# Kernel tuning notes

Measured on AMD Instinct MI355X. Metric: run time of the kernel, lower is better.

Reference implementation:

```python
import jax, jax.numpy as jnp
import numpy as np

LEAKY_ALPHA = 0.2  # LeakyReLU negative slope from init arg `alpha`


def setup_inputs() -> dict:
    key = jax.random.key(0)
    k1, k2, k3, k4 = jax.random.split(key, 4)
    B, N, Fin, Fout = 8, 2048, 256, 256
    h = jax.random.normal(k1, (B, N, Fin), dtype=jnp.float32)
    adj = jax.random.randint(k2, (N, N), 0, 2, dtype=jnp.int32)
    W = jax.random.normal(k3, (Fin, Fout), dtype=jnp.float32) * (1.414 * (6.0 / (Fin + Fout)) ** 0.5)
    a = jax.random.normal(k4, (2 * Fout, 1), dtype=jnp.float32) * (1.414 * (6.0 / (2 * Fout + 1)) ** 0.5)
    return {"h": h, "adj": adj, "W": W, "a": a}


def reference(h, adj, W, a):
    # h: (B, N, Fin), adj: (N, N) int {0,1}, W: (Fin, Fout), a: (2*Fout, 1)
    Fout = W.shape[1]
    Wh = jnp.einsum('bnf,fo->bno', h, W)            # (B, N, Fout)
    a1 = a[:Fout, 0]                                  # attends to target node i
    a2 = a[Fout:, 0]                                  # attends to source node j
    # a^T [Wh_i || Wh_j] == (Wh_i . a1) + (Wh_j . a2); LeakyReLU applied after, as in original
    s_i = Wh @ a1                                     # (B, N)
    s_j = Wh @ a2                                     # (B, N)
    e = jax.nn.leaky_relu(s_i[:, :, None] + s_j[:, None, :], negative_slope=LEAKY_ALPHA)  # (B, N, N)
    N = Wh.shape[1]
    mask = (adj > 0) | jnp.eye(N, dtype=bool)         # adjacency + self-loops
    e = jnp.where(mask[None, :, :], e, -jnp.inf)
    attention = jax.nn.softmax(e, axis=-1)            # dropout is identity in eval
    attention = jnp.nan_to_num(attention, nan=0.0)
    h_prime = jnp.einsum('bij,bjo->bio', attention, Wh)  # (B, N, Fout)
    return jax.nn.elu(h_prime)                        # concat=True -> ELU
```

## Files before the change

### kernel.cpp

```cpp
#include <hip/hip_runtime.h>

typedef unsigned short u16;
typedef unsigned int   u32;
typedef unsigned long long u64;

typedef __bf16 bf16x8 __attribute__((ext_vector_type(8)));
typedef float  f32x4  __attribute__((ext_vector_type(4)));

#define MFMA_BF16(a,b,c) __builtin_amdgcn_mfma_f32_16x16x32_bf16((a),(b),(c),0,0,0)

__device__ __forceinline__ float bf2f(u16 u) {
    return __uint_as_float(((u32)u) << 16);
}
__device__ __forceinline__ u16 f2bf(float x) {
    u32 u = __float_as_uint(x);
    u += 0x7fffu + ((u >> 16) & 1u);
    return (u16)(u >> 16);
}
__device__ __forceinline__ float ldany(const void* p, size_t i, int f32) {
    return f32 ? ((const float*)p)[i] : bf2f(((const u16*)p)[i]);
}
__device__ __forceinline__ int detect_f32(const u32* hw) {
    u32 w = hw[threadIdx.x & 63];
    int e = (w >> 23) & 0xFF;
    u64 m = __ballot(e >= 64 && e <= 190);
    return __popcll(m) >= 32 ? 1 : 0;
}

__global__ __launch_bounds__(256) void k0(const void* __restrict__ w, const void* __restrict__ a,
                                          u16* __restrict__ wt, float* __restrict__ wa1,
                                          float* __restrict__ wa2, const u32* __restrict__ hw) {
    int f32 = detect_f32(hw);
    int k = blockIdx.x, o = threadIdx.x;
    float wv = ldany(w, (size_t)k * 256 + o, f32);
    wt[o * 256 + k] = f2bf(wv);
    float p1 = wv * ldany(a, o, f32);
    float p2 = wv * ldany(a, 256 + o, f32);
    for (int d = 32; d; d >>= 1) { p1 += __shfl_down(p1, d); p2 += __shfl_down(p2, d); }
    __shared__ float s1[4], s2[4];
    int wid = o >> 6, lane = o & 63;
    if (lane == 0) { s1[wid] = p1; s2[wid] = p2; }
    __syncthreads();
    if (o == 0) { wa1[k] = s1[0] + s1[1] + s1[2] + s1[3]; wa2[k] = s2[0] + s2[1] + s2[2] + s2[3]; }
}

__global__ __launch_bounds__(256) void k1m(const int* __restrict__ adj, u64* __restrict__ mb64) {
    int t = threadIdx.x;
    int wv = t >> 6, lane = t & 63;
    #pragma unroll
    for (int q = 0; q < 4; q++) {
        int idx = blockIdx.x * 16 + wv * 4 + q;
        int mrow = idx >> 5, c = idx & 31;
        int j = c * 64 + lane;
        bool bit = (adj[(size_t)mrow * 2048 + j] > 0) || (j == mrow);
        u64 m = __ballot(bit);
        if (lane == 0) mb64[(size_t)mrow * 32 + c] = m;
    }
}

struct __align__(16) K2LDS {
    u16 At[64 * 68];
    union { u16 Bt[256 * 68]; u16 Ct[256 * 68]; };
    float wa1s[256], wa2s[256];
    float s1[64], s2[64];
};
__global__ __launch_bounds__(256) void k2(const void* __restrict__ h, const u16* __restrict__ wt,
                                          const float* __restrict__ wa1, const float* __restrict__ wa2,
                                          u16* __restrict__ whbt,
                                          float* __restrict__ sig, float* __restrict__ sjg) {
    __shared__ K2LDS L;
    int f32 = detect_f32((const u32*)h);
    int m0 = blockIdx.x * 64;
    int b  = m0 >> 11;
    int n0 = m0 & 2047;
    int t = threadIdx.x;
    int wid = t >> 6, lane = t & 63, ln = lane & 15, qd = lane >> 4;

    L.wa1s[t] = wa1[t]; L.wa2s[t] = wa2[t];
    if (t < 64) { L.s1[t] = 0.f; L.s2[t] = 0.f; }
    __syncthreads();

    float a1lo = 0.f, a2lo = 0.f, a1hi = 0.f, a2hi = 0.f;

    f32x4 acc[4][4];
    for (int mi = 0; mi < 4; mi++)
        for (int ni = 0; ni < 4; ni++)
            acc[mi][ni] = (f32x4){0.f, 0.f, 0.f, 0.f};

    for (int c = 0; c < 4; c++) {
        int k0c = c * 64;
        for (int p = 0; p < 2; p++) {
            int r = (t >> 3) + p * 32, s = t & 7;
            float xv[8]; u16 uv[8];
            if (f32) {
                const float* src = (const float*)h + (size_t)(m0 + r) * 256 + k0c + s * 8;
                f32x4 x0 = *(const f32x4*)src;
                f32x4 x1 = *(const f32x4*)(src + 4);
                #pragma unroll
                for (int q = 0; q < 4; q++) { xv[q] = x0[q]; xv[4 + q] = x1[q]; }
                #pragma unroll
                for (int q = 0; q < 8; q++) uv[q] = f2bf(xv[q]);
            } else {
                const u16* src = (const u16*)h + (size_t)(m0 + r) * 256 + k0c + s * 8;
                *(uint4*)uv = *(const uint4*)src;
                #pragma unroll
                for (int q = 0; q < 8; q++) xv[q] = bf2f(uv[q]);
            }
            *(uint4*)&L.At[r * 68 + s * 8] = *(uint4*)uv;
            float pa = 0.f, pb = 0.f;
            #pragma unroll
            for (int q = 0; q < 8; q++) {
                pa += xv[q] * L.wa1s[k0c + s * 8 + q];
                pb += xv[q] * L.wa2s[k0c + s * 8 + q];
            }
            if (p == 0) { a1lo += pa; a2lo += pb; } else { a1hi += pa; a2hi += pb; }
        }
        for (int p = 0; p < 8; p++) {
            int f = (t >> 3) + p * 32, s = t & 7;
            *(uint4*)&L.Bt[f * 68 + s * 8] =
                *(const uint4*)(wt + (size_t)f * 256 + k0c + s * 8);
        }
        __syncthreads();
        for (int ks = 0; ks < 2; ks++) {
            bf16x8 af[4], bfr[4];
            for (int mi = 0; mi < 4; mi++)
                af[mi] = *(const bf16x8*)&L.At[(mi * 16 + ln) * 68 + ks * 32 + qd * 8];
            for (int ni = 0; ni < 4; ni++)
                bfr[ni] = *(const bf16x8*)&L.Bt[(wid * 64 + ni * 16 + ln) * 68 + ks * 32 + qd * 8];
            for (int mi = 0; mi < 4; mi++)
                for (int ni = 0; ni < 4; ni++)
                    acc[mi][ni] = MFMA_BF16(af[mi], bfr[ni], acc[mi][ni]);
        }
        __syncthreads();
    }

    atomicAdd(&L.s1[t >> 3], a1lo);        atomicAdd(&L.s2[t >> 3], a2lo);
    atomicAdd(&L.s1[(t >> 3) + 32], a1hi); atomicAdd(&L.s2[(t >> 3) + 32], a2hi);

    for (int mi = 0; mi < 4; mi++) {
        for (int ni = 0; ni < 4; ni++) {
            int f = wid * 64 + ni * 16 + ln;
            int n = mi * 16 + qd * 4;
            u16 v[4];
            for (int r = 0; r < 4; r++) v[r] = f2bf(acc[mi][ni][r]);
            *(uint2*)&L.Ct[f * 68 + n] = *(uint2*)v;
        }
    }
    __syncthreads();
    if (t < 64) { sig[m0 + t] = L.s1[t]; sjg[m0 + t] = L.s2[t]; }
    {
        int fr = t;
        size_t base = (size_t)b * 524288 + (size_t)fr * 2048 + n0;
        #pragma unroll
        for (int s = 0; s < 8; s++) {
            uint4 v = *(uint4*)&L.Ct[fr * 68 + s * 8];
            *(uint4*)(whbt + base + s * 8) = v;
        }
    }
}

__global__ __launch_bounds__(512) void k3n(const float* __restrict__ sig, const float* __restrict__ sjg,
                                           float* __restrict__ u1g, float* __restrict__ u2g,
                                           u32* __restrict__ vpackg, u16* __restrict__ sjbfg) {
    int b = blockIdx.x;
    int t = threadIdx.x;
    const float* sjb = sjg + (size_t)b * 2048;
    float mx = -3.4e38f;
    #pragma unroll
    for (int p = 0; p < 4; p++) mx = fmaxf(mx, sjb[t + p * 512]);
    for (int d = 32; d; d >>= 1) mx = fmaxf(mx, __shfl_xor(mx, d));
    __shared__ float wmax[8];
    int wid = t >> 6, lane = t & 63;
    if (lane == 0) wmax[wid] = mx;
    __syncthreads();
    float Mb = fmaxf(fmaxf(fmaxf(wmax[0], wmax[1]), fmaxf(wmax[2], wmax[3])),
                     fmaxf(fmaxf(wmax[4], wmax[5]), fmaxf(wmax[6], wmax[7])));
    #pragma unroll
    for (int p = 0; p < 4; p++) {
        int j = t + p * 512;
        float sjv = sjb[j];
        float vj  = __expf(sjv - Mb);
        float v2j = __expf(0.2f * (sjv - Mb));
        vpackg[b * 2048 + j] = (u32)f2bf(vj) | ((u32)f2bf(v2j) << 16);
        sjbfg[b * 2048 + j]  = f2bf(sjv);
        float siv = sig[b * 2048 + j];
        float x = siv + Mb;
        float K = fmaxf(x, 0.2f * x);
        u1g[b * 2048 + j] = __expf(x - K);
        u2g[b * 2048 + j] = __expf(0.2f * x - K);
    }
}

struct __align__(16) K4LDS {
    u32   vpack[2048];
    u16   sjb[2048];
    u64   mw[64 * 33];
    float u1[64], u2[64], nsi[64], inv[64];
    float lred[512];
    u16   Pt[2][4096];
    int   claim[2];
};
__global__ __launch_bounds__(512, 1) void k4(const float* __restrict__ sig,
                                             const float* __restrict__ u1g, const float* __restrict__ u2g,
                                             const u32* __restrict__ vpackg, const u16* __restrict__ sjbfg,
                                             const u64* __restrict__ mb64, const u16* __restrict__ whbt,
                                             void* __restrict__ out, const void* __restrict__ hdet,
                                             int* __restrict__ cnt) {
    __shared__ K4LDS L;
    int f32 = detect_f32((const u32*)hdet);
    int t = threadIdx.x;
    if (t == 0) {
        int xcd = __builtin_amdgcn_s_getreg(63508) & 7;
        int bsel = 0, tile = 0;
        #pragma unroll
        for (int k = 0; k < 8; k++) {
            int bb = (xcd + k) & 7;
            int tt = atomicAdd(&cnt[bb], 1);
            if (tt < 32) { bsel = bb; tile = tt; break; }
        }
        L.claim[0] = bsel; L.claim[1] = tile;
    }
    __syncthreads();
    int b  = L.claim[0];
    int i0 = L.claim[1] * 64;
    int wid = t >> 6, lane = t & 63, ln = lane & 15, qd = lane >> 4;
    const u16* wb = whbt + (size_t)b * 524288 + (size_t)wid * 32 * 2048;
    float lacc = 0.f;

    bf16x8 br[2][4];
    #define LOAD_B(cc, bb) do {                                             \
        int j0_ = (cc) * 64;                                                \
        _Pragma("unroll")                                                   \
        for (int ni = 0; ni < 2; ni++)                                      \
            _Pragma("unroll")                                               \
            for (int ks = 0; ks < 2; ks++)                                  \
                br[bb][ni * 2 + ks] = *(const bf16x8*)(wb +                 \
                    (size_t)(ni * 16 + ln) * 2048 + j0_ + ks * 32 + qd * 8);\
    } while (0)

    #define PGEN(cc, bb) do {                                               \
        int r_ = lane, o_ = wid;                                            \
        int jb_ = (cc) * 64 + o_ * 8;                                       \
        uint4 pkA_ = *(const uint4*)&L.vpack[jb_];                          \
        uint4 pkB_ = *(const uint4*)&L.vpack[jb_ + 4];                      \
        uint4 sj4_ = *(const uint4*)&L.sjb[jb_];                            \
        u32 mb_ = (u32)(L.mw[r_ * 33 + (cc)] >> (o_ * 8)) & 0xffu;          \
        float u1_ = L.u1[r_], u2_ = L.u2[r_], nsi_ = L.nsi[r_];             \
        u32 pr_[4];                                                         \
        _Pragma("unroll")                                                   \
        for (int pk = 0; pk < 4; pk++) {                                    \
            u32 vw0_ = (pk == 0) ? pkA_.x : (pk == 1) ? pkA_.z              \
                     : (pk == 2) ? pkB_.x : pkB_.z;                         \
            u32 vw1_ = (pk == 0) ? pkA_.y : (pk == 1) ? pkA_.w              \
                     : (pk == 2) ? pkB_.y : pkB_.w;                         \
            u32 sw_ = (pk == 0) ? sj4_.x : (pk == 1) ? sj4_.y               \
                     : (pk == 2) ? sj4_.z : sj4_.w;                         \
            float sj0_ = __uint_as_float(sw_ << 16);                        \
            float sj1_ = __uint_as_float(sw_ & 0xffff0000u);                \
            float p0_, p1_;                                                 \
            {                                                               \
                bool pos = sj0_ > nsi_;                                     \
                float vv = __uint_as_float(pos ? (vw0_ << 16)               \
                                               : ((vw0_ >> 16) << 16));     \
                p0_ = (pos ? u1_ : u2_) * vv;                               \
                p0_ = ((mb_ >> (2 * pk)) & 1u) ? p0_ : 0.f;                 \
            }                                                               \
            {                                                               \
                bool pos = sj1_ > nsi_;                                     \
                float vv = __uint_as_float(pos ? (vw1_ << 16)               \
                                               : ((vw1_ >> 16) << 16));     \
                p1_ = (pos ? u1_ : u2_) * vv;                               \
                p1_ = ((mb_ >> (2 * pk + 1)) & 1u) ? p1_ : 0.f;             \
            }                                                               \
            lacc += p0_ + p1_;                                              \
            pr_[pk] = __builtin_amdgcn_perm(__float_as_uint(p1_),           \
                                            __float_as_uint(p0_),           \
                                            0x07060302u);                   \
        }                                                                   \
        *(uint4*)&L.Pt[bb][t * 8] = *(uint4*)pr_;                           \
    } while (0)

    LOAD_B(0, 0);
    for (int p = 0; p < 4; p++) { int idx = t + p * 512; L.vpack[idx] = vpackg[b * 2048 + idx]; }
    for (int p = 0; p < 2; p++) { int idx = t + p * 512;
        ((u32*)L.sjb)[idx] = ((const u32*)(sjbfg + (size_t)b * 2048))[idx]; }
    for (int p = 0; p < 4; p++) {
        int idx = t + p * 512;
        int r = idx >> 5, c = idx & 31;
        L.mw[r * 33 + c] = mb64[(size_t)(i0 + r) * 32 + c];
    }
    if (t < 64) {
        int row = b * 2048 + i0 + t;
        L.u1[t] = u1g[row]; L.u2[t] = u2g[row]; L.nsi[t] = -sig[row];
    }
    __syncthreads();
    PGEN(0, 0);

    f32x4 acc[4][2];
    for (int mi = 0; mi < 4; mi++)
        for (int ni = 0; ni < 2; ni++)
            acc[mi][ni] = (f32x4){0.f, 0.f, 0.f, 0.f};

    #define STEP(c, cur, nxt) do {                                          \
        __syncthreads();                                                    \
        if ((c) < 31) { LOAD_B((c) + 1, nxt); PGEN((c) + 1, nxt); }         \
        _Pragma("unroll")                                                   \
        for (int ks = 0; ks < 2; ks++) {                                    \
            bf16x8 af[4];                                                   \
            _Pragma("unroll")                                               \
            for (int mi = 0; mi < 4; mi++)                                  \
                af[mi] = *(const bf16x8*)&L.Pt[cur][((ks * 4 + qd) * 64 +   \
                                                     mi * 16 + ln) * 8];    \
            _Pragma("unroll")                                               \
            for (int mi = 0; mi < 4; mi++)                                  \
                _Pragma("unroll")                                           \
                for (int ni = 0; ni < 2; ni++)                              \
                    acc[mi][ni] = MFMA_BF16(af[mi], br[cur][ni * 2 + ks],   \
                                            acc[mi][ni]);                   \
        }                                                                   \
    } while (0)

    for (int cc = 0; cc < 16; cc++) {
        STEP(2 * cc,     0, 1);
        STEP(2 * cc + 1, 1, 0);
    }

    __syncthreads();
    L.lred[t] = lacc;
    __syncthreads();
    if (t < 64) {
        float s = 0.f;
        #pragma unroll
        for (int q = 0; q < 8; q++) s += L.lred[q * 64 + t];
        L.inv[t] = 1.0f / s;
    }
    __syncthreads();

    for (int mi = 0; mi < 4; mi++) {
        for (int ni = 0; ni < 2; ni++) {
            int fg = wid * 32 + ni * 16 + ln;
            for (int reg = 0; reg < 4; reg++) {
                int rl = mi * 16 + qd * 4 + reg;
                float hp = acc[mi][ni][reg] * L.inv[rl];
                float y = hp > 0.f ? hp : (__expf(hp) - 1.f);
                size_t idx = (size_t)(b * 2048 + i0 + rl) * 256 + fg;
                if (f32) ((float*)out)[idx] = y;
                else     ((u16*)out)[idx]   = f2bf(y);
            }
        }
    }
    #undef LOAD_B
    #undef PGEN
    #undef STEP
}

extern "C" void kernel_launch(void* const* d_in, const int* in_sizes, int n_in,
                              void* d_out, int out_size, void* d_ws, size_t ws_size,
                              hipStream_t stream) {
    const void* h   = d_in[0];
    const int*  adj = (const int*)d_in[1];
    const void* W   = d_in[2];
    const void* a   = d_in[3];

    char* ws = (char*)d_ws;
    u16*   WT    = (u16*)  (ws + 0);
    float* si    = (float*)(ws + 131072);
    float* sj    = (float*)(ws + 196608);
    float* u1    = (float*)(ws + 262144);
    float* u2    = (float*)(ws + 327680);
    u32*   vpack = (u32*)  (ws + 458752);
    u16*   sjbf  = (u16*)  (ws + 524288);
    u64*   mb64  = (u64*)  (ws + 557056);
    u16*   whbt  = (u16*)  (ws + 1081344);
    float* Wa1   = (float*)(ws + 9469952);
    float* Wa2   = (float*)(ws + 9470976);
    int*   cnt   = (int*)  (ws + 9472000);

    hipMemsetAsync(cnt, 0, 32, stream);
    k0 <<<dim3(256),  dim3(256), 0, stream>>>(W, a, WT, Wa1, Wa2, (const u32*)h);
    k1m<<<dim3(4096), dim3(256), 0, stream>>>(adj, mb64);
    k2 <<<dim3(256),  dim3(256), 0, stream>>>(h, WT, Wa1, Wa2, whbt, si, sj);
    k3n<<<dim3(8),    dim3(512), 0, stream>>>(si, sj, u1, u2, vpack, sjbf);
    k4 <<<dim3(256),  dim3(512), 0, stream>>>(si, u1, u2, vpack, sjbf, mb64, whbt, d_out, h, cnt);
}
```

Baseline: 140.0 us.

## Use 16 waves per attention block with 128-wide column chunks and MFMA priority

The fused attention-aggregation kernel moves from 8 to 16 waves per block. Each wave now owns 16 output features instead of 32, and each pipeline step covers 128 source columns instead of 64, which halves the number of barrier-separated steps. Probability generation is spread over 1024 threads, and s_setprio raises wave priority around the MFMA section. The aim is more latency hiding and fewer syncs, at the cost of double the LDS staging for P, fewer MFMAs per B-fragment load, and possibly tighter register limits.

Measured after the change: 139.7 us. No clear change (-0.2%).

```diff
diff --git a/kernel.cpp b/kernel.cpp
--- a/kernel.cpp
+++ b/kernel.cpp
@@ -196,16 +196,16 @@
     u16   sjb[2048];
     u64   mw[64 * 33];
     float u1[64], u2[64], nsi[64], inv[64];
-    float lred[512];
-    u16   Pt[2][4096];
+    float lred[1024];
+    u16   Pt[2][8192];
     int   claim[2];
 };
-__global__ __launch_bounds__(512, 1) void k4(const float* __restrict__ sig,
-                                             const float* __restrict__ u1g, const float* __restrict__ u2g,
-                                             const u32* __restrict__ vpackg, const u16* __restrict__ sjbfg,
-                                             const u64* __restrict__ mb64, const u16* __restrict__ whbt,
-                                             void* __restrict__ out, const void* __restrict__ hdet,
-                                             int* __restrict__ cnt) {
+__global__ __launch_bounds__(1024, 4) void k4(const float* __restrict__ sig,
+                                              const float* __restrict__ u1g, const float* __restrict__ u2g,
+                                              const u32* __restrict__ vpackg, const u16* __restrict__ sjbfg,
+                                              const u64* __restrict__ mb64, const u16* __restrict__ whbt,
+                                              void* __restrict__ out, const void* __restrict__ hdet,
+                                              int* __restrict__ cnt) {
     __shared__ K4LDS L;
     int f32 = detect_f32((const u32*)hdet);
     int t = threadIdx.x;
@@ -224,27 +224,26 @@
     int b  = L.claim[0];
     int i0 = L.claim[1] * 64;
     int wid = t >> 6, lane = t & 63, ln = lane & 15, qd = lane >> 4;
-    const u16* wb = whbt + (size_t)b * 524288 + (size_t)wid * 32 * 2048;
+    const u16* wb = whbt + (size_t)b * 524288 + (size_t)wid * 16 * 2048;
     float lacc = 0.f;
 
     bf16x8 br[2][4];
     #define LOAD_B(cc, bb) do {                                             \
-        int j0_ = (cc) * 64;                                                \
+        int j0_ = (cc) * 128;                                               \
         _Pragma("unroll")                                                   \
-        for (int ni = 0; ni < 2; ni++)                                      \
-            _Pragma("unroll")                                               \
-            for (int ks = 0; ks < 2; ks++)                                  \
-                br[bb][ni * 2 + ks] = *(const bf16x8*)(wb +                 \
-                    (size_t)(ni * 16 + ln) * 2048 + j0_ + ks * 32 + qd * 8);\
+        for (int ks = 0; ks < 4; ks++)                                      \
+            br[bb][ks] = *(const bf16x8*)(wb +                              \
+                (size_t)ln * 2048 + j0_ + ks * 32 + qd * 8);                \
     } while (0)
 
     #define PGEN(cc, bb) do {                                               \
-        int r_ = lane, o_ = wid;                                            \
-        int jb_ = (cc) * 64 + o_ * 8;                                       \
+        int r_ = t & 63, o_ = t >> 6;                                       \
+        int jb_ = (cc) * 128 + o_ * 8;                                      \
         uint4 pkA_ = *(const uint4*)&L.vpack[jb_];                          \
         uint4 pkB_ = *(const uint4*)&L.vpack[jb_ + 4];                      \
         uint4 sj4_ = *(const uint4*)&L.sjb[jb_];                            \
-        u32 mb_ = (u32)(L.mw[r_ * 33 + (cc)] >> (o_ * 8)) & 0xffu;          \
+        u32 mb_ = (u32)(L.mw[r_ * 33 + 2 * (cc) + (o_ >> 3)]                \
+                        >> ((o_ & 7) * 8)) & 0xffu;                         \
         float u1_ = L.u1[r_], u2_ = L.u2[r_], nsi_ = L.nsi[r_];             \
         u32 pr_[4];                                                         \
         _Pragma("unroll")                                                   \
@@ -281,11 +280,10 @@
     } while (0)
 
     LOAD_B(0, 0);
-    for (int p = 0; p < 4; p++) { int idx = t + p * 512; L.vpack[idx] = vpackg[b * 2048 + idx]; }
-    for (int p = 0; p < 2; p++) { int idx = t + p * 512;
-        ((u32*)L.sjb)[idx] = ((const u32*)(sjbfg + (size_t)b * 2048))[idx]; }
-    for (int p = 0; p < 4; p++) {
-        int idx = t + p * 512;
+    for (int p = 0; p < 2; p++) { int idx = t + p * 1024; L.vpack[idx] = vpackg[b * 2048 + idx]; }
+    ((u32*)L.sjb)[t] = ((const u32*)(sjbfg + (size_t)b * 2048))[t];
+    for (int p = 0; p < 2; p++) {
+        int idx = t + p * 1024;
         int r = idx >> 5, c = idx & 31;
         L.mw[r * 33 + c] = mb64[(size_t)(i0 + r) * 32 + c];
     }
@@ -296,16 +294,16 @@
     __syncthreads();
     PGEN(0, 0);
 
-    f32x4 acc[4][2];
+    f32x4 acc[4];
     for (int mi = 0; mi < 4; mi++)
-        for (int ni = 0; ni < 2; ni++)
-            acc[mi][ni] = (f32x4){0.f, 0.f, 0.f, 0.f};
+        acc[mi] = (f32x4){0.f, 0.f, 0.f, 0.f};
 
     #define STEP(c, cur, nxt) do {                                          \
         __syncthreads();                                                    \
-        if ((c) < 31) { LOAD_B((c) + 1, nxt); PGEN((c) + 1, nxt); }         \
+        if ((c) < 15) { LOAD_B((c) + 1, nxt); PGEN((c) + 1, nxt); }         \
+        __builtin_amdgcn_s_setprio(1);                                      \
         _Pragma("unroll")                                                   \
-        for (int ks = 0; ks < 2; ks++) {                                    \
+        for (int ks = 0; ks < 4; ks++) {                                    \
             bf16x8 af[4];                                                   \
             _Pragma("unroll")                                               \
             for (int mi = 0; mi < 4; mi++)                                  \
@@ -313,14 +311,12 @@
                                                      mi * 16 + ln) * 8];    \
             _Pragma("unroll")                                               \
             for (int mi = 0; mi < 4; mi++)                                  \
-                _Pragma("unroll")                                           \
-                for (int ni = 0; ni < 2; ni++)                              \
-                    acc[mi][ni] = MFMA_BF16(af[mi], br[cur][ni * 2 + ks],   \
-                                            acc[mi][ni]);                   \
+                acc[mi] = MFMA_BF16(af[mi], br[cur][ks], acc[mi]);          \
         }                                                                   \
+        __builtin_amdgcn_s_setprio(0);                                      \
     } while (0)
 
-    for (int cc = 0; cc < 16; cc++) {
+    for (int cc = 0; cc < 8; cc++) {
         STEP(2 * cc,     0, 1);
         STEP(2 * cc + 1, 1, 0);
     }
@@ -331,17 +327,17 @@
     if (t < 64) {
         float s = 0.f;
         #pragma unroll
-        for (int q = 0; q < 8; q++) s += L.lred[q * 64 + t];
+        for (int q = 0; q < 16; q++) s += L.lred[q * 64 + t];
         L.inv[t] = 1.0f / s;
     }
     __syncthreads();
 
-    for (int mi = 0; mi < 4; mi++) {
-        for (int ni = 0; ni < 2; ni++) {
-            int fg = wid * 32 + ni * 16 + ln;
+    {
+        int fg = wid * 16 + ln;
+        for (int mi = 0; mi < 4; mi++) {
             for (int reg = 0; reg < 4; reg++) {
                 int rl = mi * 16 + qd * 4 + reg;
-                float hp = acc[mi][ni][reg] * L.inv[rl];
+                float hp = acc[mi][reg] * L.inv[rl];
                 float y = hp > 0.f ? hp : (__expf(hp) - 1.f);
                 size_t idx = (size_t)(b * 2048 + i0 + rl) * 256 + fg;
                 if (f32) ((float*)out)[idx] = y;
@@ -381,5 +377,5 @@
     k1m<<<dim3(4096), dim3(256), 0, stream>>>(adj, mb64);
     k2 <<<dim3(256),  dim3(256), 0, stream>>>(h, WT, Wa1, Wa2, whbt, si, sj);
     k3n<<<dim3(8),    dim3(512), 0, stream>>>(si, sj, u1, u2, vpack, sjbf);
-    k4 <<<dim3(256),  dim3(512), 0, stream>>>(si, u1, u2, vpack, sjbf, mb64, whbt, d_out, h, cnt);
-}
+    k4 <<<dim3(256),  dim3(1024), 0, stream>>>(si, u1, u2, vpack, sjbf, mb64, whbt, d_out, h, cnt);
+}
```
